# Optimization experiments

Measured on AMD Instinct MI355X. Metric: run time of the kernel, lower is better.

Reference implementation:

```python
import jax, jax.numpy as jnp
import numpy as np

B, S, D = 2, 1024, 4096
H, KV, HD = 32, 8, 128
GROUP = H // KV


def qlinear(x, w_int8, w_scale, bias):
    """Int8 dynamic-activation-quant linear: per-row activation scale, per-out-channel weight scale."""
    K = x.shape[-1]
    xf = x.reshape(-1, K)
    sx = jnp.max(jnp.abs(xf), axis=1, keepdims=True) / 127.0  # [M,1]
    sx = jnp.where(sx == 0, jnp.float32(1.0), sx)
    xi = jax.lax.stop_gradient(jnp.clip(jnp.round(xf / sx), -127.0, 127.0)).astype(jnp.int8)
    y = jnp.matmul(xi.astype(jnp.int32), w_int8.T.astype(jnp.int32)).astype(jnp.float32)  # int32 accum
    y = y * sx * w_scale[None, :]
    if bias is not None:
        y = y + bias
    return y.reshape(x.shape[:-1] + (w_int8.shape[0],))


def rope(t, c, s):
    half = t.shape[-1] // 2
    rot = jnp.concatenate([-t[..., half:], t[..., :half]], axis=-1)
    return t * c + rot * s


def setup_inputs() -> dict:
    key = jax.random.key(0)
    ks = jax.random.split(key, 10)
    x = jax.random.normal(ks[0], (B, S, D), dtype=jnp.float32)
    # RoPE tables (full-head_dim rotate-half convention)
    inv = 1.0 / (10000.0 ** (jnp.arange(0, HD, 2, dtype=jnp.float32) / HD))
    ang = jnp.arange(S, dtype=jnp.float32)[:, None] * inv[None, :]  # [S, HD/2]
    cos = jnp.concatenate([jnp.cos(ang), jnp.cos(ang)], axis=-1)
    sin = jnp.concatenate([jnp.sin(ang), jnp.sin(ang)], axis=-1)
    d_kv = KV * HD
    wq = jax.random.randint(ks[1], (H * HD, D), -127, 128, dtype=jnp.int32).astype(jnp.int8)
    wk = jax.random.randint(ks[2], (d_kv, D), -127, 128, dtype=jnp.int32).astype(jnp.int8)
    wv = jax.random.randint(ks[3], (d_kv, D), -127, 128, dtype=jnp.int32).astype(jnp.int8)
    wo = jax.random.randint(ks[4], (D, H * HD), -127, 128, dtype=jnp.int32).astype(jnp.int8)
    sc_in = jnp.float32(1.0 / (127.0 * np.sqrt(D)))
    sc_o = jnp.float32(1.0 / (127.0 * np.sqrt(H * HD)))
    sq = jnp.full((H * HD,), sc_in, dtype=jnp.float32)
    sk = jnp.full((d_kv,), sc_in, dtype=jnp.float32)
    sv = jnp.full((d_kv,), sc_in, dtype=jnp.float32)
    so = jnp.full((D,), sc_o, dtype=jnp.float32)
    bq = 0.01 * jax.random.normal(ks[5], (H * HD,), dtype=jnp.float32)
    bk = 0.01 * jax.random.normal(ks[6], (d_kv,), dtype=jnp.float32)
    bv = 0.01 * jax.random.normal(ks[7], (d_kv,), dtype=jnp.float32)
    return {"x": x, "cos": cos, "sin": sin, "wq": wq, "sq": sq, "bq": bq,
            "wk": wk, "sk": sk, "bk": bk, "wv": wv, "sv": sv, "bv": bv,
            "wo": wo, "so": so}


def reference(x, cos, sin, wq, sq, bq, wk, sk, bk, wv, sv, bv, wo, so):
    b, seq, _ = x.shape
    q = qlinear(x, wq, sq, bq).reshape(b, seq, H, HD)
    k = qlinear(x, wk, sk, bk).reshape(b, seq, KV, HD)
    v = qlinear(x, wv, sv, bv).reshape(b, seq, KV, HD)
    c = cos[:seq][None, :, None, :]
    s = sin[:seq][None, :, None, :]
    q = rope(q, c, s)
    k = rope(k, c, s)
    # start_pos=0 prefill: cache write then slice-back is identity -> use k, v directly.
    # GQA broadcast: q_head_to_kv_head = h // group_size
    idx = jnp.arange(H) // GROUP
    kf = k[:, :, idx, :]  # [b, seq, H, HD]
    vf = v[:, :, idx, :]
    scores = jnp.einsum('bqhd,bkhd->bhqk', q, kf) / jnp.sqrt(jnp.float32(HD))
    causal = jnp.tril(jnp.ones((seq, seq), dtype=bool))
    scores = jnp.where(causal[None, None, :, :], scores, jnp.float32(-jnp.inf))
    probs = jax.nn.softmax(scores, axis=-1)
    out = jnp.einsum('bhqk,bkhd->bqhd', probs, vf).reshape(b, seq, H * HD)
    return qlinear(out, wo, so, None)
```

## Files before the change

### kernel.cpp

```cpp
#include <hip/hip_runtime.h>


#define B_   2
#define S_   1024
#define D_   4096
#define H_   32
#define KV_  8
#define HD_  128
#define NR   (B_ * S_)
#define NQKV (H_*HD_ + 2*KV_*HD_)

typedef __attribute__((ext_vector_type(8))) short  short8;
typedef __attribute__((ext_vector_type(4))) short  short4v;
typedef __attribute__((ext_vector_type(4))) float  f32x4;
typedef __attribute__((ext_vector_type(4))) int    int4v;

#define FA_SW(c, r) (((c) & 8) | (((c) & 7) ^ ((r) & 7)))

static __device__ __forceinline__ unsigned short f2bf(float f) {
    unsigned u = __builtin_bit_cast(unsigned, f);
    u += 0x7fffu + ((u >> 16) & 1u);
    return (unsigned short)(u >> 16);
}

static __device__ __forceinline__ void async_cp16(const void* g, void* l) {
    __builtin_amdgcn_global_load_lds(
        (const __attribute__((address_space(1))) void*)g,
        (__attribute__((address_space(3))) void*)l, 16, 0, 0);
}

__global__ __launch_bounds__(256) void quantize_rows_k(
    const float* __restrict__ X, signed char* __restrict__ Xq,
    float* __restrict__ sx_out)
{
    int row = blockIdx.x;
    const f32x4* xr = (const f32x4*)(X + (size_t)row * 4096);
    int t = threadIdx.x;

    f32x4 v[4];
    #pragma unroll
    for (int i = 0; i < 4; i++) v[i] = xr[t + i * 256];

    float m = 0.f;
    #pragma unroll
    for (int i = 0; i < 4; i++)
        #pragma unroll
        for (int j = 0; j < 4; j++) m = fmaxf(m, fabsf(v[i][j]));
    #pragma unroll
    for (int off = 32; off > 0; off >>= 1) m = fmaxf(m, __shfl_down(m, off, 64));
    __shared__ float red[4];
    if ((t & 63) == 0) red[t >> 6] = m;
    __syncthreads();
    float mm = fmaxf(fmaxf(red[0], red[1]), fmaxf(red[2], red[3]));
    float sx = mm / 127.0f;
    if (sx == 0.f) sx = 1.f;
    if (t == 0) sx_out[row] = sx;

    int* dst = (int*)(Xq + (size_t)row * 4096);
    #pragma unroll
    for (int i = 0; i < 4; i++) {
        int o = 0;
        #pragma unroll
        for (int j = 0; j < 4; j++) {
            float q = rintf(v[i][j] / sx);
            q = fminf(fmaxf(q, -127.f), 127.f);
            o |= (((int)q) & 0xff) << (j * 8);
        }
        dst[t + i * 256] = o;
    }
}

__global__ __launch_bounds__(256) void convert_all_w(
    const int* __restrict__ wq, const int* __restrict__ wk,
    const int* __restrict__ wv, const int* __restrict__ wo,
    signed char* __restrict__ Wqkv, signed char* __restrict__ Wo)
{
    int tid = blockIdx.x * 256 + threadIdx.x;
    #pragma unroll
    for (int it = 0; it < 20; ++it) {
        int i = tid + it * 524288;
        const int* src;
        int* dst;
        if (i < 4194304)      { src = wq + (size_t)i * 4;              dst = (int*)Wqkv + i; }
        else if (i < 5242880) { int j = i - 4194304; src = wk + (size_t)j * 4; dst = (int*)(Wqkv + 16777216) + j; }
        else if (i < 6291456) { int j = i - 5242880; src = wv + (size_t)j * 4; dst = (int*)(Wqkv + 20971520) + j; }
        else                  { int j = i - 6291456; src = wo + (size_t)j * 4; dst = (int*)Wo + j; }
        int4v a = *(const int4v*)src;
        *dst = (a[0] & 0xff) | ((a[1] & 0xff) << 8) | ((a[2] & 0xff) << 16) | (a[3] << 24);
    }
}

template<int MODE>
__global__ __launch_bounds__(256) void gemm_i8_k(
    const signed char* __restrict__ A, const signed char* __restrict__ Bm,
    float* __restrict__ C, const float* __restrict__ rs,
    const float* __restrict__ cs, int K, int lda, int ldb, int ldc)
{
    __shared__ __align__(16) signed char As[128 * 128];
    __shared__ __align__(16) signed char Bs[128 * 128];

    int t    = threadIdx.x;
    int m0   = blockIdx.y * 128;
    int n0   = blockIdx.x * 128;
    int lane = t & 63;
    int w    = t >> 6;
    int wm   = (w >> 1) * 64;
    int wn   = (w & 1) * 64;
    int l15  = lane & 15;
    int quad = lane >> 4;

    int4v acc[4][4];
    #pragma unroll
    for (int i = 0; i < 4; i++)
        #pragma unroll
        for (int j = 0; j < 4; j++) { int4v z = {0,0,0,0}; acc[i][j] = z; }

    int cw   = w * 64 + lane;
    int smr  = cw >> 3;
    int scol = cw & 7;

    for (int k0 = 0; k0 < K; k0 += 128) {
        #pragma unroll
        for (int p = 0; p < 4; ++p) {
            int m  = p * 32 + smr;
            int kc = scol ^ (m & 7);
            const signed char* ga = A  + (size_t)(m0 + m) * lda + k0 + kc * 16;
            const signed char* gb = Bm + (size_t)(n0 + m) * ldb + k0 + kc * 16;
            async_cp16(ga, As + (p * 256 + w * 64) * 16);
            async_cp16(gb, Bs + (p * 256 + w * 64) * 16);
        }
        __syncthreads();

        #pragma unroll
        for (int ks = 0; ks < 2; ks++) {
            int4v af[4], bf[4];
            #pragma unroll
            for (int i = 0; i < 4; i++) {
                int ra = wm + i*16 + l15;
                int rb = wn + i*16 + l15;
                af[i] = *(const int4v*)&As[(ra * 8 + (((ks*4 + quad) ^ (ra & 7)))) * 16];
                bf[i] = *(const int4v*)&Bs[(rb * 8 + (((ks*4 + quad) ^ (rb & 7)))) * 16];
            }
            #pragma unroll
            for (int i = 0; i < 4; i++)
                #pragma unroll
                for (int j = 0; j < 4; j++)
                    acc[i][j] = __builtin_amdgcn_mfma_i32_16x16x64_i8(af[i], bf[j], acc[i][j], 0, 0, 0);
        }
        __syncthreads();
    }

    #pragma unroll
    for (int i = 0; i < 4; i++) {
        #pragma unroll
        for (int j = 0; j < 4; j++) {
            #pragma unroll
            for (int r = 0; r < 4; r++) {
                int row = m0 + wm + i*16 + quad*4 + r;
                int col = n0 + wn + j*16 + l15;
                float v = (float)acc[i][j][r];
                if (MODE == 3) v *= rs[row] * cs[col];
                C[(size_t)row * ldc + col] = v;
            }
        }
    }
}

__global__ __launch_bounds__(256) void derope_k(
    const float* __restrict__ Y, const float* __restrict__ sx,
    const float* __restrict__ sq, const float* __restrict__ bq,
    const float* __restrict__ sk, const float* __restrict__ bk,
    const float* __restrict__ cosb, const float* __restrict__ sinb,
    unsigned short* __restrict__ Q, unsigned short* __restrict__ Kb)
{
    const float qs = 0.08838834764831845f;
    int r = blockIdx.x;
    int b = r >> 10;
    int s = r & (S_ - 1);
    float sxr = sx[r];
    const float* yr = Y + (size_t)r * NQKV;
    int t = threadIdx.x;

    for (int p = t; p < H_ * 64; p += 256) {
        int h = p >> 6, d = p & 63;
        int ca = h * HD_ + d;
        float a  = yr[ca]      * sxr * sq[ca]      + bq[ca];
        float b2 = yr[ca + 64] * sxr * sq[ca + 64] + bq[ca + 64];
        float c  = cosb[s * HD_ + d], sn = sinb[s * HD_ + d];
        size_t base = (((size_t)(b * H_ + h)) * S_ + s) * HD_;
        Q[base + d]      = f2bf((a * c - b2 * sn) * qs);
        Q[base + d + 64] = f2bf((b2 * c + a * sn) * qs);
    }
    for (int p = t; p < KV_ * 64; p += 256) {
        int kv = p >> 6, d = p & 63;
        int ci = kv * HD_ + d;
        int ca = H_ * HD_ + ci;
        float a  = yr[ca]      * sxr * sk[ci]      + bk[ci];
        float b2 = yr[ca + 64] * sxr * sk[ci + 64] + bk[ci + 64];
        float c  = cosb[s * HD_ + d], sn = sinb[s * HD_ + d];
        size_t base = (((size_t)(b * KV_ + kv)) * S_ + s) * HD_;
        Kb[base + d]      = f2bf(a * c - b2 * sn);
        Kb[base + d + 64] = f2bf(b2 * c + a * sn);
    }
}

__global__ __launch_bounds__(256) void vtrans_k(
    const float* __restrict__ Y, const float* __restrict__ sx,
    const float* __restrict__ sv, const float* __restrict__ bv,
    unsigned short* __restrict__ Vt)
{
    __shared__ float lds[64 * 129];

    int bkv = blockIdx.x;
    int b   = bkv >> 3;
    int kv  = bkv & 7;
    int s0  = blockIdx.y * 64;
    int t   = threadIdx.x;
    const int vcol = H_ * HD_ + KV_ * HD_ + kv * HD_;

    #pragma unroll
    for (int i = 0; i < 8; ++i) {
        int idx = t + i * 256;
        int sl  = idx >> 5;
        int dq  = (idx & 31) * 4;
        int row = b * S_ + s0 + sl;
        f32x4 y4 = *(const f32x4*)(Y + (size_t)row * NQKV + vcol + dq);
        f32x4 s4 = *(const f32x4*)(sv + kv * HD_ + dq);
        f32x4 b4 = *(const f32x4*)(bv + kv * HD_ + dq);
        float sxr = sx[row];
        #pragma unroll
        for (int j = 0; j < 4; ++j)
            lds[sl * 129 + dq + j] = y4[j] * sxr * s4[j] + b4[j];
    }
    __syncthreads();

    unsigned short* Vb = Vt + ((size_t)(b * KV_ + kv)) * (HD_ * S_);
    #pragma unroll
    for (int i = 0; i < 8; ++i) {
        int idx = t + i * 256;
        int hd  = idx >> 4;
        int ss  = (idx & 15) * 4;
        short4v ov;
        #pragma unroll
        for (int j = 0; j < 4; ++j)
            ov[j] = (short)f2bf(lds[(ss + j) * 129 + hd]);
        *(short4v*)&Vb[(size_t)hd * S_ + s0 + ss] = ov;
    }
}

__global__ __launch_bounds__(256, 2) void flash_attn_k(
    const unsigned short* __restrict__ Qg,
    const unsigned short* __restrict__ Kg,
    const unsigned short* __restrict__ Vg,
    float* __restrict__ O)
{
    __shared__ __align__(16) unsigned short Ks[128 * 128];
    __shared__ __align__(16) unsigned short Vs[128 * 128];

    int pair = blockIdx.x;
    int tp   = blockIdx.y;
    int b    = pair >> 5;
    int kv   = (pair & 31) >> 2;

    const unsigned short* Kbp = Kg + ((size_t)(b * KV_ + kv)) * (S_ * HD_);
    const unsigned short* Vb  = Vg + ((size_t)(b * KV_ + kv)) * (HD_ * S_);

    int t    = threadIdx.x;
    int lane = t & 63;
    int w    = t >> 6;
    int l15  = lane & 15;
    int quad = lane >> 4;
    int trow = t >> 4;
    int tcol = t & 15;

    short8 kreg[8], vreg[8];
    #pragma unroll
    for (int p = 0; p < 8; ++p) {
        int row = p * 16 + trow;
        kreg[p] = *(const short8*)(Kbp + (size_t)row * HD_ + tcol * 8);
        vreg[p] = *(const short8*)(Vb  + (size_t)row * S_  + tcol * 8);
    }

    #pragma unroll
    for (int phase = 0; phase < 2; ++phase) {
        int qt   = phase ? (15 - tp) : tp;
        int n128 = (qt + 2) >> 1;
        const unsigned short* Qb = Qg + ((size_t)pair * S_ + qt * 64) * HD_;

        short8 qf[4];
        #pragma unroll
        for (int ks = 0; ks < 4; ks++)
            qf[ks] = *(const short8*)(Qb + (size_t)(w*16 + l15) * HD_ + ks*32 + quad*8);

        f32x4 oacc[8];
        #pragma unroll
        for (int n = 0; n < 8; n++) { f32x4 z = {0.f,0.f,0.f,0.f}; oacc[n] = z; }
        float mrow[4], lrow[4];
        #pragma unroll
        for (int r = 0; r < 4; r++) { mrow[r] = -1e30f; lrow[r] = 0.f; }

        for (int j = 0; j < n128; ++j) {
            __syncthreads();

            #pragma unroll
            for (int p = 0; p < 8; ++p) {
                int row = p * 16 + trow;
                int c = FA_SW(tcol, row);
                *(short8*)&Ks[row * 128 + c * 8] = kreg[p];
                *(short8*)&Vs[row * 128 + c * 8] = vreg[p];
            }
            __syncthreads();

            int k0n = (j + 1 < n128) ? (j + 1) * 128 : (phase == 0 ? 0 : -1);
            if (k0n >= 0) {
                #pragma unroll
                for (int p = 0; p < 8; ++p) {
                    int row = p * 16 + trow;
                    kreg[p] = *(const short8*)(Kbp + (size_t)(k0n + row) * HD_ + tcol * 8);
                    vreg[p] = *(const short8*)(Vb  + (size_t)row * S_ + k0n + tcol * 8);
                }
            }

            f32x4 sacc[8];
            #pragma unroll
            for (int n = 0; n < 8; n++) { f32x4 z = {0.f,0.f,0.f,0.f}; sacc[n] = z; }
            #pragma unroll
            for (int n = 0; n < 8; n++) {
                int row = n*16 + l15;
                #pragma unroll
                for (int ks = 0; ks < 4; ks++) {
                    short8 kf = *(const short8*)&Ks[row * 128 + FA_SW(ks*4 + quad, row) * 8];
                    sacc[n] = __builtin_amdgcn_mfma_f32_16x16x32_bf16(qf[ks], kf, sacc[n], 0, 0, 0);
                }
            }

            if (j == n128 - 1) {
                int k0 = j * 128;
                #pragma unroll
                for (int n = 0; n < 8; n++)
                    #pragma unroll
                    for (int r = 0; r < 4; r++) {
                        int kcol = k0 + n*16 + l15;
                        int qrow = qt*64 + w*16 + quad*4 + r;
                        if (kcol > qrow) sacc[n][r] = -1e30f;
                    }
            }

            #pragma unroll
            for (int r = 0; r < 4; r++) {
                float mx = sacc[0][r];
                #pragma unroll
                for (int n = 1; n < 8; n++) mx = fmaxf(mx, sacc[n][r]);
                mx = fmaxf(mx, __shfl_xor(mx, 1, 64));
                mx = fmaxf(mx, __shfl_xor(mx, 2, 64));
                mx = fmaxf(mx, __shfl_xor(mx, 4, 64));
                mx = fmaxf(mx, __shfl_xor(mx, 8, 64));
                float mnew = fmaxf(mrow[r], mx);
                float alpha = __expf(mrow[r] - mnew);
                mrow[r] = mnew;
                float s = 0.f;
                #pragma unroll
                for (int n = 0; n < 8; n++) {
                    float e = __expf(sacc[n][r] - mnew);
                    sacc[n][r] = e;
                    s += e;
                }
                s += __shfl_xor(s, 1, 64);
                s += __shfl_xor(s, 2, 64);
                s += __shfl_xor(s, 4, 64);
                s += __shfl_xor(s, 8, 64);
                lrow[r] = lrow[r] * alpha + s;
                #pragma unroll
                for (int n = 0; n < 8; n++) oacc[n][r] *= alpha;
            }

            __syncthreads();

            #pragma unroll
            for (int n = 0; n < 8; n++)
                #pragma unroll
                for (int r = 0; r < 4; r++) {
                    int qrow = w*16 + quad*4 + r;
                    int kcol = n*16 + l15;
                    Ks[qrow * 128 + FA_SW(kcol >> 3, qrow) * 8 + (kcol & 7)] = f2bf(sacc[n][r]);
                }

            short8 pf[4];
            #pragma unroll
            for (int ks = 0; ks < 4; ks++) {
                int row = w*16 + l15;
                pf[ks] = *(const short8*)&Ks[row * 128 + FA_SW(ks*4 + quad, row) * 8];
            }
            #pragma unroll
            for (int n = 0; n < 8; n++) {
                int row = n*16 + l15;
                #pragma unroll
                for (int ks = 0; ks < 4; ks++) {
                    short8 vf = *(const short8*)&Vs[row * 128 + FA_SW(ks*4 + quad, row) * 8];
                    oacc[n] = __builtin_amdgcn_mfma_f32_16x16x32_bf16(pf[ks], vf, oacc[n], 0, 0, 0);
                }
            }
        }

        float* Ob = O + ((size_t)(b * S_ + qt * 64)) * (H_*HD_) + (pair & 31) * HD_;
        #pragma unroll
        for (int r = 0; r < 4; r++) {
            float inv = 1.0f / lrow[r];
            int row = w*16 + quad*4 + r;
            #pragma unroll
            for (int n = 0; n < 8; n++)
                Ob[(size_t)row * (H_*HD_) + n*16 + l15] = oacc[n][r] * inv;
        }
    }
}

extern "C" void kernel_launch(void* const* d_in, const int* in_sizes, int n_in,
                              void* d_out, int out_size, void* d_ws, size_t ws_size,
                              hipStream_t stream)
{
    (void)in_sizes; (void)n_in; (void)out_size; (void)ws_size;
    const float* x    = (const float*)d_in[0];
    const float* cosb = (const float*)d_in[1];
    const float* sinb = (const float*)d_in[2];
    const int*   wq   = (const int*)d_in[3];
    const float* sq   = (const float*)d_in[4];
    const float* bq   = (const float*)d_in[5];
    const int*   wk   = (const int*)d_in[6];
    const float* sk   = (const float*)d_in[7];
    const float* bk   = (const float*)d_in[8];
    const int*   wv   = (const int*)d_in[9];
    const float* sv   = (const float*)d_in[10];
    const float* bv   = (const float*)d_in[11];
    const int*   wo   = (const int*)d_in[12];
    const float* so   = (const float*)d_in[13];
    float* out = (float*)d_out;
    char*  ws  = (char*)d_ws;

    signed char*    Xi   = (signed char*)(ws + 0);
    float*          Y    = (float*)(ws + 8388608ull);
    signed char*    Wqkv = (signed char*)(ws + 58720256ull);
    signed char*    Oi   = (signed char*)(ws + 58720256ull);
    signed char*    Wo   = (signed char*)(ws + 83886080ull);
    unsigned short* Q    = (unsigned short*)(ws + 100663296ull);
    unsigned short* Kb   = (unsigned short*)(ws + 117440512ull);
    unsigned short* Vt   = (unsigned short*)(ws + 121634816ull);
    float*          O    = (float*)(ws + 125829120ull);
    float*          sx   = (float*)(ws + 159383552ull);
    float*          sxo  = (float*)(ws + 159391744ull);

    quantize_rows_k<<<dim3(NR), dim3(256), 0, stream>>>(x, Xi, sx);

    convert_all_w<<<dim3(2048), dim3(256), 0, stream>>>(wq, wk, wv, wo, Wqkv, Wo);

    gemm_i8_k<0><<<dim3(48,16,1), dim3(256), 0, stream>>>(
        Xi, Wqkv, Y, nullptr, nullptr, D_, D_, D_, NQKV);

    derope_k<<<dim3(NR), dim3(256), 0, stream>>>(
        Y, sx, sq, bq, sk, bk, cosb, sinb, Q, Kb);

    vtrans_k<<<dim3(B_*KV_, S_/64), dim3(256), 0, stream>>>(Y, sx, sv, bv, Vt);

    flash_attn_k<<<dim3(64, 8), dim3(256), 0, stream>>>(Q, Kb, Vt, O);

    quantize_rows_k<<<dim3(NR), dim3(256), 0, stream>>>(O, Oi, sxo);

    gemm_i8_k<3><<<dim3(32,16,1), dim3(256), 0, stream>>>(
        Oi, Wo, out, sxo, so, D_, D_, D_, D_);
}
```

Baseline: 404.5 us.

## Fuse weight conversion with input quantization; use separate P buffer in attention

Merges the int32-to-int8 weight conversion and the activation row quantization into one launch, with the first blocks converting weights and the rest quantizing rows. This removes a kernel launch and lets the two memory-bound jobs overlap. The flash attention kernel gets a dedicated LDS buffer for the probability tile, so the barrier before writing P can go. Oi is moved to the Y region so it no longer aliases the weight buffer. The extra 16KB of LDS may lower attention occupancy, and the conversion loop now runs 40 iterations per thread.

```diff
diff --git a/kernel.cpp b/kernel.cpp
--- a/kernel.cpp
+++ b/kernel.cpp
@@ -10,6 +10,8 @@
 #define NR   (B_ * S_)
 #define NQKV (H_*HD_ + 2*KV_*HD_)
 
+#define CONV_BLKS 1024
+
 typedef __attribute__((ext_vector_type(8))) short  short8;
 typedef __attribute__((ext_vector_type(4))) short  short4v;
 typedef __attribute__((ext_vector_type(4))) float  f32x4;
@@ -29,13 +31,35 @@
         (__attribute__((address_space(3))) void*)l, 16, 0, 0);
 }
 
-__global__ __launch_bounds__(256) void quantize_rows_k(
+__global__ __launch_bounds__(256) void prep_k(
     const float* __restrict__ X, signed char* __restrict__ Xq,
-    float* __restrict__ sx_out)
-{
-    int row = blockIdx.x;
+    float* __restrict__ sx_out,
+    const int* __restrict__ wq, const int* __restrict__ wk,
+    const int* __restrict__ wv, const int* __restrict__ wo,
+    signed char* __restrict__ Wqkv, signed char* __restrict__ Wo)
+{
+    int bx = blockIdx.x;
+    int t  = threadIdx.x;
+
+    if (bx < CONV_BLKS) {
+        int tid = bx * 256 + t;
+        #pragma unroll
+        for (int it = 0; it < 40; ++it) {
+            int i = tid + it * 262144;
+            const int* src;
+            int* dst;
+            if (i < 4194304)      { src = wq + (size_t)i * 4;              dst = (int*)Wqkv + i; }
+            else if (i < 5242880) { int j = i - 4194304; src = wk + (size_t)j * 4; dst = (int*)(Wqkv + 16777216) + j; }
+            else if (i < 6291456) { int j = i - 5242880; src = wv + (size_t)j * 4; dst = (int*)(Wqkv + 20971520) + j; }
+            else                  { int j = i - 6291456; src = wo + (size_t)j * 4; dst = (int*)Wo + j; }
+            int4v a = *(const int4v*)src;
+            *dst = (a[0] & 0xff) | ((a[1] & 0xff) << 8) | ((a[2] & 0xff) << 16) | (a[3] << 24);
+        }
+        return;
+    }
+
+    int row = bx - CONV_BLKS;
     const f32x4* xr = (const f32x4*)(X + (size_t)row * 4096);
-    int t = threadIdx.x;
 
     f32x4 v[4];
     #pragma unroll
@@ -70,23 +94,44 @@
     }
 }
 
-__global__ __launch_bounds__(256) void convert_all_w(
-    const int* __restrict__ wq, const int* __restrict__ wk,
-    const int* __restrict__ wv, const int* __restrict__ wo,
-    signed char* __restrict__ Wqkv, signed char* __restrict__ Wo)
-{
-    int tid = blockIdx.x * 256 + threadIdx.x;
-    #pragma unroll
-    for (int it = 0; it < 20; ++it) {
-        int i = tid + it * 524288;
-        const int* src;
-        int* dst;
-        if (i < 4194304)      { src = wq + (size_t)i * 4;              dst = (int*)Wqkv + i; }
-        else if (i < 5242880) { int j = i - 4194304; src = wk + (size_t)j * 4; dst = (int*)(Wqkv + 16777216) + j; }
-        else if (i < 6291456) { int j = i - 5242880; src = wv + (size_t)j * 4; dst = (int*)(Wqkv + 20971520) + j; }
-        else                  { int j = i - 6291456; src = wo + (size_t)j * 4; dst = (int*)Wo + j; }
-        int4v a = *(const int4v*)src;
-        *dst = (a[0] & 0xff) | ((a[1] & 0xff) << 8) | ((a[2] & 0xff) << 16) | (a[3] << 24);
+__global__ __launch_bounds__(256) void quantize_rows_k(
+    const float* __restrict__ X, signed char* __restrict__ Xq,
+    float* __restrict__ sx_out)
+{
+    int row = blockIdx.x;
+    const f32x4* xr = (const f32x4*)(X + (size_t)row * 4096);
+    int t = threadIdx.x;
+
+    f32x4 v[4];
+    #pragma unroll
+    for (int i = 0; i < 4; i++) v[i] = xr[t + i * 256];
+
+    float m = 0.f;
+    #pragma unroll
+    for (int i = 0; i < 4; i++)
+        #pragma unroll
+        for (int j = 0; j < 4; j++) m = fmaxf(m, fabsf(v[i][j]));
+    #pragma unroll
+    for (int off = 32; off > 0; off >>= 1) m = fmaxf(m, __shfl_down(m, off, 64));
+    __shared__ float red[4];
+    if ((t & 63) == 0) red[t >> 6] = m;
+    __syncthreads();
+    float mm = fmaxf(fmaxf(red[0], red[1]), fmaxf(red[2], red[3]));
+    float sx = mm / 127.0f;
+    if (sx == 0.f) sx = 1.f;
+    if (t == 0) sx_out[row] = sx;
+
+    int* dst = (int*)(Xq + (size_t)row * 4096);
+    #pragma unroll
+    for (int i = 0; i < 4; i++) {
+        int o = 0;
+        #pragma unroll
+        for (int j = 0; j < 4; j++) {
+            float q = rintf(v[i][j] / sx);
+            q = fminf(fmaxf(q, -127.f), 127.f);
+            o |= (((int)q) & 0xff) << (j * 8);
+        }
+        dst[t + i * 256] = o;
     }
 }
 
@@ -256,6 +301,7 @@
 {
     __shared__ __align__(16) unsigned short Ks[128 * 128];
     __shared__ __align__(16) unsigned short Vs[128 * 128];
+    __shared__ __align__(16) unsigned short Ps[64 * 128];
 
     int pair = blockIdx.x;
     int tp   = blockIdx.y;
@@ -374,22 +420,20 @@
                 for (int n = 0; n < 8; n++) oacc[n][r] *= alpha;
             }
 
-            __syncthreads();
-
             #pragma unroll
             for (int n = 0; n < 8; n++)
                 #pragma unroll
                 for (int r = 0; r < 4; r++) {
                     int qrow = w*16 + quad*4 + r;
                     int kcol = n*16 + l15;
-                    Ks[qrow * 128 + FA_SW(kcol >> 3, qrow) * 8 + (kcol & 7)] = f2bf(sacc[n][r]);
+                    Ps[qrow * 128 + FA_SW(kcol >> 3, qrow) * 8 + (kcol & 7)] = f2bf(sacc[n][r]);
                 }
 
             short8 pf[4];
             #pragma unroll
             for (int ks = 0; ks < 4; ks++) {
                 int row = w*16 + l15;
-                pf[ks] = *(const short8*)&Ks[row * 128 + FA_SW(ks*4 + quad, row) * 8];
+                pf[ks] = *(const short8*)&Ps[row * 128 + FA_SW(ks*4 + quad, row) * 8];
             }
             #pragma unroll
             for (int n = 0; n < 8; n++) {
@@ -438,8 +482,8 @@
 
     signed char*    Xi   = (signed char*)(ws + 0);
     float*          Y    = (float*)(ws + 8388608ull);
+    signed char*    Oi   = (signed char*)(ws + 8388608ull);
     signed char*    Wqkv = (signed char*)(ws + 58720256ull);
-    signed char*    Oi   = (signed char*)(ws + 58720256ull);
     signed char*    Wo   = (signed char*)(ws + 83886080ull);
     unsigned short* Q    = (unsigned short*)(ws + 100663296ull);
     unsigned short* Kb   = (unsigned short*)(ws + 117440512ull);
@@ -448,9 +492,8 @@
     float*          sx   = (float*)(ws + 159383552ull);
     float*          sxo  = (float*)(ws + 159391744ull);
 
-    quantize_rows_k<<<dim3(NR), dim3(256), 0, stream>>>(x, Xi, sx);
-
-    convert_all_w<<<dim3(2048), dim3(256), 0, stream>>>(wq, wk, wv, wo, Wqkv, Wo);
+    prep_k<<<dim3(CONV_BLKS + NR), dim3(256), 0, stream>>>(
+        x, Xi, sx, wq, wk, wv, wo, Wqkv, Wo);
 
     gemm_i8_k<0><<<dim3(48,16,1), dim3(256), 0, stream>>>(
         Xi, Wqkv, Y, nullptr, nullptr, D_, D_, D_, NQKV);
```

After: 402.8 us. No clear change (-0.4%).
